# Performance work log

Hardware: AMD Instinct MI355X
Metric: run time of the kernel (lower is better)

Reference implementation:

```python
import jax, jax.numpy as jnp
import numpy as np
import math

D, H, F = 1024, 16, 4096
DH = D // H
EPS_LN = 1e-5


def _layernorm(x, scale, bias):
    mu = jnp.mean(x, axis=-1, keepdims=True)
    var = jnp.mean(jnp.square(x - mu), axis=-1, keepdims=True)
    return (x - mu) * jax.lax.rsqrt(var + EPS_LN) * scale + bias


def setup_inputs() -> dict:
    key = jax.random.key(0)
    ks = jax.random.split(key, 16)
    B, T = 2, 2048
    src = jax.random.normal(ks[0], (B, T, D), dtype=jnp.float32)
    attn_mask = jax.random.randint(ks[1], (T, T), 0, 2) == 1  # bool [T,S], True = masked
    xavier = lambda k, shp: jax.random.uniform(k, shp, jnp.float32, -1.0, 1.0) * math.sqrt(6.0 / (shp[0] + shp[1]))
    return {
        "src": src, "attn_mask": attn_mask,
        "q_w": xavier(ks[2], (D, D)), "q_b": jnp.zeros((D,), jnp.float32),
        "k_w": xavier(ks[3], (D, D)), "k_b": jnp.zeros((D,), jnp.float32),
        "v_w": xavier(ks[4], (D, D)), "v_b": jnp.zeros((D,), jnp.float32),
        "o_w": xavier(ks[5], (D, D)), "o_b": jnp.zeros((D,), jnp.float32),
        "l1_w": xavier(ks[6], (F, D)), "l1_b": jnp.zeros((F,), jnp.float32),
        "l2_w": xavier(ks[7], (D, F)), "l2_b": jnp.zeros((D,), jnp.float32),
        "n1_s": jnp.ones((D,), jnp.float32), "n1_b": jnp.zeros((D,), jnp.float32),
        "n2_s": jnp.ones((D,), jnp.float32), "n2_b": jnp.zeros((D,), jnp.float32),
        "alpha_attn": jax.random.normal(ks[8], (), jnp.float32) * 0.1,
        "alpha_ff": jax.random.normal(ks[9], (), jnp.float32) * 0.1,
    }


def reference(src, attn_mask, q_w, q_b, k_w, k_b, v_w, v_b, o_w, o_b,
              l1_w, l1_b, l2_w, l2_b, n1_s, n1_b, n2_s, n2_b,
              alpha_attn, alpha_ff):
    B, T, _ = src.shape
    # --- self-attention block (post-norm layer, dropout=0 => identity) ---
    q = (src @ q_w.T + q_b).reshape(B, T, H, DH).transpose(0, 2, 1, 3)  # [B,H,T,DH]
    k = (src @ k_w.T + k_b).reshape(B, T, H, DH).transpose(0, 2, 1, 3)
    v = (src @ v_w.T + v_b).reshape(B, T, H, DH).transpose(0, 2, 1, 3)
    scores = jnp.einsum('bhtd,bhsd->bhts', q, k) / math.sqrt(DH)  # [B,H,T,S]
    scores = jnp.where(attn_mask[None, None, :, :], -jnp.inf, scores)
    probs = jax.nn.softmax(scores + 1e-9, axis=-1)
    probs = jnp.where(jnp.isinf(scores), 0.0, probs)  # zero where masked (custom semantics)
    attn = jnp.einsum('bhts,bhsd->bhtd', probs, v).transpose(0, 2, 1, 3).reshape(B, T, D)
    attn = attn @ o_w.T + o_b
    x = _layernorm(src + alpha_attn * attn, n1_s, n1_b)
    # --- FFN block ---
    ff = jax.nn.relu(x @ l1_w.T + l1_b) @ l2_w.T + l2_b
    x = _layernorm(x + alpha_ff * ff, n2_s, n2_b)
    return x
```

## Files before the change

### kernel.cpp

```cpp
#include <hip/hip_runtime.h>
#include <math.h>

#define Dm 1024
#define Hh 16
#define DHd 64
#define Ff 4096
#define Tt 2048
#define Bb 2

#define ATT_C2 0.18033688011112042f

typedef __bf16 bf16_8 __attribute__((ext_vector_type(8)));
typedef __bf16 bf16x2 __attribute__((ext_vector_type(2)));
typedef __bf16 bf16x4 __attribute__((ext_vector_type(4)));
typedef float  f32x4  __attribute__((ext_vector_type(4)));
typedef float  f32x16 __attribute__((ext_vector_type(16)));
typedef unsigned int u32x4 __attribute__((ext_vector_type(4)));
typedef unsigned int u32x8s __attribute__((ext_vector_type(8)));

__device__ __forceinline__ unsigned short f2bf(float f) {
    unsigned int u = __float_as_uint(f);
    unsigned int r = (u + 0x7fffu + ((u >> 16) & 1u)) >> 16;
    return (unsigned short)r;
}

__device__ __forceinline__ bf16x2 pkbf(float a, float b) {
#if __has_builtin(__builtin_amdgcn_cvt_pk_bf16_f32)
    return __builtin_amdgcn_cvt_pk_bf16_f32(a, b);
#else
    bf16x2 r; r[0] = (__bf16)a; r[1] = (__bf16)b; return r;
#endif
}
__device__ __forceinline__ bf16x4 pkbf4(float a, float b, float c, float d) {
    bf16x2 lo = pkbf(a, b), hi = pkbf(c, d);
    return __builtin_shufflevector(lo, hi, 0, 1, 2, 3);
}

__device__ __forceinline__ void plswap32(unsigned &a, unsigned &b) {
#if __has_builtin(__builtin_amdgcn_permlane32_swap)
    auto r = __builtin_amdgcn_permlane32_swap((int)a, (int)b, false, false);
    a = (unsigned)r[0]; b = (unsigned)r[1];
#else
    asm volatile("v_permlane32_swap_b32 %0, %1" : "+v"(a), "+v"(b));
#endif
}

__device__ __forceinline__ void gld_lds16(const void* g, void* l) {
    __builtin_amdgcn_global_load_lds(
        (const __attribute__((address_space(1))) void*)g,
        (__attribute__((address_space(3))) void*)l,
        16, 0, 0);
}

__device__ __forceinline__ void sload32(const unsigned* p,
        u32x8s &a, u32x8s &b, u32x8s &c, u32x8s &d) {
    asm volatile(
        "s_load_dwordx8 %0, %4, 0x0\n\t"
        "s_load_dwordx8 %1, %4, 0x20\n\t"
        "s_load_dwordx8 %2, %4, 0x40\n\t"
        "s_load_dwordx8 %3, %4, 0x60\n\t"
        "s_waitcnt lgkmcnt(0)"
        : "=s"(a), "=s"(b), "=s"(c), "=s"(d)
        : "s"(p));
}

__device__ __forceinline__ float selkeep(float e, unsigned long long keep) {
    float r;
    asm("v_cndmask_b32 %0, 0, %1, %2" : "=v"(r) : "v"(e), "s"(keep));
    return r;
}

__global__ __launch_bounds__(256) void preprocess_kernel(
    const float* __restrict__ q_w, const float* __restrict__ k_w,
    const float* __restrict__ v_w, const float* __restrict__ o_w,
    const float* __restrict__ l1_w, const float* __restrict__ l2_w,
    const float* __restrict__ src, const int* __restrict__ mask,
    const float* __restrict__ q_b, const float* __restrict__ k_b,
    unsigned short* __restrict__ qkw, unsigned short* __restrict__ vw16,
    unsigned short* __restrict__ ow,  unsigned short* __restrict__ l1w,
    unsigned short* __restrict__ l2w, unsigned short* __restrict__ srcb,
    unsigned* __restrict__ mbT, float* __restrict__ qkb)
{
    const int bid = blockIdx.x;
    const int tid = threadIdx.x;
    if (bid < 16384) {
        int i = bid * 256 + tid;
        const float* sp; unsigned short* dp; int off;
        if (i < 1048576) {
            if (i < 262144)      { sp = q_w; dp = qkw;           off = i; }
            else if (i < 524288) { sp = k_w; dp = qkw + 1048576; off = i - 262144; }
            else if (i < 786432) { sp = v_w; dp = vw16;          off = i - 524288; }
            else                 { sp = o_w; dp = ow;            off = i - 786432; }
        } else if (i < 2097152)  { sp = l1_w; dp = l1w;          off = i - 1048576; }
        else if (i < 3145728)    { sp = l2_w; dp = l2w;          off = i - 2097152; }
        else                     { sp = src;  dp = srcb;         off = i - 3145728; }
        float4 v = ((const float4*)sp)[off];
        ((bf16x4*)dp)[off] = pkbf4(v.x, v.y, v.z, v.w);
    } else if (bid < 16896) {
        int w = (bid - 16384) * 256 + tid;
        int tw32 = w >> 11, s = w & 2047;
        const int* p = mask + (size_t)(tw32 * 32) * 2048 + s;
        unsigned bits = 0;
        #pragma unroll
        for (int j = 0; j < 32; ++j)
            bits |= (p[(size_t)j * 2048] == 0 ? 1u : 0u) << j;
        mbT[w] = bits;
    } else {
        int i = (bid - 16896) * 256 + tid;
        qkb[i] = (i < 1024) ? q_b[i] : k_b[i - 1024];
    }
}

template<int RELU, int BF16OUT>
__global__ __launch_bounds__(256) void gemm_bf16_kernel(
    const unsigned short* __restrict__ A, const unsigned short* __restrict__ W,
    const float* __restrict__ bias, void* __restrict__ C, void* __restrict__ C2,
    int M, int N, int K, int ldc, int ksub)
{
    __shared__ __bf16 As[128][64];
    __shared__ __bf16 Bs[128][64];
    const int tid  = threadIdx.x;
    const int lane = tid & 63;
    const int wave = tid >> 6;
    const int m0 = blockIdx.y * 128;
    const int n0 = blockIdx.x * 128;
    const int lr8 = lane >> 3;
    const int gch = (lane & 7) ^ lr8;
    const int wm = (wave & 1) * 64;
    const int wn = (wave >> 1) * 64;
    const int quad = lane >> 4;
    const int lm = lane & 15;
    const int z  = blockIdx.z;
    const int kstart = z * ksub;
    void* Cz = (z == 0) ? C : C2;

    f32x4 acc[4][4];
    #pragma unroll
    for (int i = 0; i < 4; i++)
        #pragma unroll
        for (int j = 0; j < 4; j++) {
            acc[i][j][0] = 0.f; acc[i][j][1] = 0.f;
            acc[i][j][2] = 0.f; acc[i][j][3] = 0.f;
        }

    for (int k0 = kstart; k0 < kstart + ksub; k0 += 64) {
        __syncthreads();
        #pragma unroll
        for (int i = 0; i < 4; i++) {
            int seg = wave * 4 + i;
            int r = seg * 8 + lr8;
            gld_lds16(A + (size_t)(m0 + r) * K + k0 + gch * 8, &As[seg * 8][0]);
            gld_lds16(W + (size_t)(n0 + r) * K + k0 + gch * 8, &Bs[seg * 8][0]);
        }
        __syncthreads();
        #pragma unroll
        for (int kh = 0; kh < 2; kh++) {
            bf16_8 af[4], bfr[4];
            #pragma unroll
            for (int t = 0; t < 4; t++) {
                int ch = (kh * 4 + quad) ^ (lm & 7);
                af[t]  = *(const bf16_8*)&As[wm + t * 16 + lm][ch * 8];
                bfr[t] = *(const bf16_8*)&Bs[wn + t * 16 + lm][ch * 8];
            }
            #pragma unroll
            for (int i = 0; i < 4; i++)
                #pragma unroll
                for (int j = 0; j < 4; j++)
                    acc[i][j] = __builtin_amdgcn_mfma_f32_16x16x32_bf16(
                        af[i], bfr[j], acc[i][j], 0, 0, 0);
        }
    }

    float bvc[4];
    #pragma unroll
    for (int j = 0; j < 4; j++)
        bvc[j] = (z == 0) ? bias[n0 + wn + j * 16 + lm] : 0.f;

    #pragma unroll
    for (int i = 0; i < 4; i++)
        #pragma unroll
        for (int j = 0; j < 4; j++) {
            int col = n0 + wn + j * 16 + lm;
            #pragma unroll
            for (int r = 0; r < 4; r++) {
                int row = m0 + wm + i * 16 + quad * 4 + r;
                float v = acc[i][j][r] + bvc[j];
                if (RELU) v = fmaxf(v, 0.f);
                if (BF16OUT)
                    ((unsigned short*)Cz)[(size_t)row * ldc + col] = f2bf(v);
                else
                    ((float*)Cz)[(size_t)row * ldc + col] = v;
            }
        }
}

__global__ __launch_bounds__(256, 2) void gemm_ffn1_kernel(
    const unsigned short* __restrict__ A, const unsigned short* __restrict__ W,
    const float* __restrict__ bias, unsigned short* __restrict__ C)
{
    __shared__ __bf16 As[256][64];
    __shared__ __bf16 Bs[128][64];
    const int tid  = threadIdx.x;
    const int lane = tid & 63;
    const int wave = tid >> 6;
    const int m0 = blockIdx.y * 256;
    const int n0 = blockIdx.x * 128;
    const int lr8 = lane >> 3;
    const int gch = (lane & 7) ^ lr8;
    const int quad = lane >> 4;
    const int lm = lane & 15;

    f32x4 acc[4][8];
    #pragma unroll
    for (int i = 0; i < 4; i++)
        #pragma unroll
        for (int j = 0; j < 8; j++) {
            acc[i][j][0] = 0.f; acc[i][j][1] = 0.f;
            acc[i][j][2] = 0.f; acc[i][j][3] = 0.f;
        }

    for (int k0 = 0; k0 < 1024; k0 += 64) {
        __syncthreads();
        #pragma unroll
        for (int i = 0; i < 8; i++) {
            int seg = wave * 8 + i;
            int r = seg * 8 + lr8;
            gld_lds16(A + (size_t)(m0 + r) * 1024 + k0 + gch * 8, &As[seg * 8][0]);
        }
        #pragma unroll
        for (int i = 0; i < 4; i++) {
            int seg = wave * 4 + i;
            int r = seg * 8 + lr8;
            gld_lds16(W + (size_t)(n0 + r) * 1024 + k0 + gch * 8, &Bs[seg * 8][0]);
        }
        __syncthreads();
        #pragma unroll
        for (int kh = 0; kh < 2; kh++) {
            const int ch = (kh * 4 + quad) ^ (lm & 7);
            bf16_8 af[4], bfr[8];
            #pragma unroll
            for (int t = 0; t < 4; t++)
                af[t] = *(const bf16_8*)&As[wave * 64 + t * 16 + lm][ch * 8];
            #pragma unroll
            for (int j = 0; j < 8; j++)
                bfr[j] = *(const bf16_8*)&Bs[j * 16 + lm][ch * 8];
            #pragma unroll
            for (int i = 0; i < 4; i++)
                #pragma unroll
                for (int j = 0; j < 8; j++)
                    acc[i][j] = __builtin_amdgcn_mfma_f32_16x16x32_bf16(
                        af[i], bfr[j], acc[i][j], 0, 0, 0);
        }
    }

    float bv[8];
    #pragma unroll
    for (int j = 0; j < 8; j++) bv[j] = bias[n0 + j * 16 + lm];

    #pragma unroll
    for (int i = 0; i < 4; i++)
        #pragma unroll
        for (int j = 0; j < 8; j++) {
            int col = n0 + j * 16 + lm;
            #pragma unroll
            for (int r = 0; r < 4; r++) {
                int row = m0 + wave * 64 + i * 16 + quad * 4 + r;
                float v = fmaxf(acc[i][j][r] + bv[j], 0.f);
                C[(size_t)row * Ff + col] = f2bf(v);
            }
        }
}

__global__ __launch_bounds__(256) void gemm_qkvt_kernel(
    const unsigned short* __restrict__ srcb, const unsigned short* __restrict__ qkw,
    const unsigned short* __restrict__ vw16, const float* __restrict__ qkb,
    const float* __restrict__ v_b,
    unsigned short* __restrict__ qk16, unsigned short* __restrict__ vtf)
{
    const int bid = blockIdx.x;
    const unsigned short *A, *W;
    const float* bias;
    unsigned short* C;
    int m0, n0, ldc;
    bool qscale, rowbias;
    if (bid < 512) {
        A = srcb; W = qkw; bias = qkb; C = qk16;
        n0 = (bid & 15) * 128; m0 = (bid >> 4) * 128;
        ldc = 2048; qscale = true; rowbias = false;
    } else {
        int b2 = bid - 512;
        A = vw16; W = srcb; bias = v_b; C = vtf;
        n0 = (b2 & 31) * 128; m0 = (b2 >> 5) * 128;
        ldc = 4096; qscale = false; rowbias = true;
    }
    const int K = 1024;

    __shared__ __bf16 As[128][64];
    __shared__ __bf16 Bs[128][64];
    const int tid  = threadIdx.x;
    const int lane = tid & 63;
    const int wave = tid >> 6;
    const int lr8 = lane >> 3;
    const int gch = (lane & 7) ^ lr8;
    const int wm = (wave & 1) * 64;
    const int wn = (wave >> 1) * 64;
    const int quad = lane >> 4;
    const int lm = lane & 15;

    f32x4 acc[4][4];
    #pragma unroll
    for (int i = 0; i < 4; i++)
        #pragma unroll
        for (int j = 0; j < 4; j++) {
            acc[i][j][0] = 0.f; acc[i][j][1] = 0.f;
            acc[i][j][2] = 0.f; acc[i][j][3] = 0.f;
        }

    for (int k0 = 0; k0 < K; k0 += 64) {
        __syncthreads();
        #pragma unroll
        for (int i = 0; i < 4; i++) {
            int seg = wave * 4 + i;
            int r = seg * 8 + lr8;
            gld_lds16(A + (size_t)(m0 + r) * K + k0 + gch * 8, &As[seg * 8][0]);
            gld_lds16(W + (size_t)(n0 + r) * K + k0 + gch * 8, &Bs[seg * 8][0]);
        }
        __syncthreads();
        #pragma unroll
        for (int kh = 0; kh < 2; kh++) {
            bf16_8 af[4], bfr[4];
            #pragma unroll
            for (int t = 0; t < 4; t++) {
                int ch = (kh * 4 + quad) ^ (lm & 7);
                af[t]  = *(const bf16_8*)&As[wm + t * 16 + lm][ch * 8];
                bfr[t] = *(const bf16_8*)&Bs[wn + t * 16 + lm][ch * 8];
            }
            #pragma unroll
            for (int i = 0; i < 4; i++)
                #pragma unroll
                for (int j = 0; j < 4; j++)
                    acc[i][j] = __builtin_amdgcn_mfma_f32_16x16x32_bf16(
                        af[i], bfr[j], acc[i][j], 0, 0, 0);
        }
    }

    float bvc[4];
    float brr[4][4];
    if (!rowbias) {
        #pragma unroll
        for (int j = 0; j < 4; j++) bvc[j] = bias[n0 + wn + j * 16 + lm];
    } else {
        #pragma unroll
        for (int i = 0; i < 4; i++) {
            float4 t4 = *(const float4*)&bias[m0 + wm + i * 16 + quad * 4];
            brr[i][0] = t4.x; brr[i][1] = t4.y; brr[i][2] = t4.z; brr[i][3] = t4.w;
        }
    }

    #pragma unroll
    for (int i = 0; i < 4; i++)
        #pragma unroll
        for (int j = 0; j < 4; j++) {
            int col = n0 + wn + j * 16 + lm;
            #pragma unroll
            for (int r = 0; r < 4; r++) {
                int row = m0 + wm + i * 16 + quad * 4 + r;
                float v = acc[i][j][r] + (rowbias ? brr[i][r] : bvc[j]);
                if (qscale && col < 1024) v *= ATT_C2;
                C[(size_t)row * ldc + col] = f2bf(v);
            }
        }
}

__global__ __launch_bounds__(256) void attn_mfma_kernel(
    const unsigned short* __restrict__ qk,
    const unsigned short* __restrict__ vt,
    const unsigned* __restrict__ mbT,
    unsigned short* __restrict__ out)
{
    __shared__ __bf16 Ks[2][128 * 64];
    __shared__ __bf16 Vt[2][64 * 128];

    const int tid  = threadIdx.x;
    const int lane = tid & 63;
    const int wave = tid >> 6;
    const int l31  = lane & 31;
    const int hi   = lane >> 5;
    const int x7   = l31 & 7;
    const int bh = blockIdx.y;
    const int b = bh >> 4, h = bh & 15;
    const int tw = blockIdx.x * 128 + wave * 32;
    const int wvu = __builtin_amdgcn_readfirstlane(wave);
    const unsigned* mrow = mbT + (size_t)(blockIdx.x * 4 + wvu) * 2048;

    bf16_8 qf[4];
    #pragma unroll
    for (int ds4 = 0; ds4 < 4; ++ds4)
        qf[ds4] = *(const bf16_8*)(qk +
            (size_t)(b * Tt + tw + l31) * 2048 + h * DHd + ds4 * 16 + hi * 8);

    f32x16 oacc[2];
    f32x16 ol;
    f32x16 z16;
    #pragma unroll
    for (int r = 0; r < 16; ++r) {
        oacc[0][r] = 0.f; oacc[1][r] = 0.f; ol[r] = 0.f; z16[r] = 0.f;
    }
    bf16_8 vone;
    {
        __bf16 one = (__bf16)1.0f;
        #pragma unroll
        for (int j = 0; j < 8; ++j) vone[j] = one;
    }

    const int krow8 = lane >> 3;
    const int kj    = (lane & 7) ^ krow8;
    const int vr4   = lane >> 4;

    auto STAGE = [&](int nb, int s0) {
        #pragma unroll
        for (int i = 0; i < 4; ++i) {
            int ci = wave * 4 + i;
            {
                int r = 8 * ci + krow8;
                const unsigned short* g = qk +
                    (size_t)(b * Tt + s0 + r) * 2048 + 1024 + h * DHd + kj * 8;
                gld_lds16(g, &Ks[nb][ci * 512]);
            }
            {
                int d = 4 * ci + vr4;
                int jj = (lane & 15) ^ (d & 7);
                const unsigned short* g = vt +
                    (size_t)(h * DHd + d) * 4096 + b * Tt + s0 + jj * 8;
                gld_lds16(g, &Vt[nb][ci * 512]);
            }
        }
    };

    STAGE(0, 0);

    for (int st = 0; st < 16; ++st) {
        const int cb = st & 1;
        const int s0 = st * 128;
        __syncthreads();

        if (st < 15) STAGE(cb ^ 1, s0 + 128);

        #pragma unroll
        for (int sb = 0; sb < 4; ++sb) {
            u32x8s ma, mbw, mc, md;
            sload32(mrow + s0 + sb * 32, ma, mbw, mc, md);

            f32x16 sacc = z16;
            #pragma unroll
            for (int ds4 = 0; ds4 < 4; ++ds4) {
                bf16_8 kf = *(const bf16_8*)&Ks[cb][
                    (sb * 32 + l31) * 64 + (((ds4 * 2 + hi) ^ x7) * 8)];
                sacc = __builtin_amdgcn_mfma_f32_32x32x16_bf16(
                    kf, qf[ds4], sacc, 0, 0, 0);
            }
            float p[16];
            #pragma unroll
            for (int g = 0; g < 4; ++g) {
                u32x8s vv = (g == 0) ? ma : (g == 1) ? mbw : (g == 2) ? mc : md;
                #pragma unroll
                for (int m = 0; m < 4; ++m) {
                    const int reg = g * 4 + m;
                    unsigned long long keep =
                        ((unsigned long long)vv[m + 4] << 32) |
                        (unsigned long long)vv[m];
                    float e = __builtin_amdgcn_exp2f(sacc[reg]);
                    p[reg] = selkeep(e, keep);
                }
            }
            unsigned u[4], v[4];
            #pragma unroll
            for (int g = 0; g < 4; ++g) {
                u[g] = __builtin_bit_cast(unsigned, pkbf(p[g * 4 + 0], p[g * 4 + 1]));
                v[g] = __builtin_bit_cast(unsigned, pkbf(p[g * 4 + 2], p[g * 4 + 3]));
            }
            plswap32(u[0], u[1]); plswap32(v[0], v[1]);
            plswap32(u[2], u[3]); plswap32(v[2], v[3]);
            u32x4 w0; w0[0] = u[0]; w0[1] = v[0]; w0[2] = u[1]; w0[3] = v[1];
            u32x4 w1; w1[0] = u[2]; w1[1] = v[2]; w1[2] = u[3]; w1[3] = v[3];
            bf16_8 pa0 = __builtin_bit_cast(bf16_8, w0);
            bf16_8 pa1 = __builtin_bit_cast(bf16_8, w1);
            #pragma unroll
            for (int kst = 0; kst < 2; ++kst) {
                bf16_8 pa = kst ? pa1 : pa0;
                #pragma unroll
                for (int dblk = 0; dblk < 2; ++dblk) {
                    int cpos = (sb * 4 + kst * 2 + hi) ^ x7;
                    bf16_8 vf = *(const bf16_8*)&Vt[cb][
                        ((dblk * 32 + l31) * 16 + cpos) * 8];
                    oacc[dblk] = __builtin_amdgcn_mfma_f32_32x32x16_bf16(
                        pa, vf, oacc[dblk], 0, 0, 0);
                }
                ol = __builtin_amdgcn_mfma_f32_32x32x16_bf16(
                    pa, vone, ol, 0, 0, 0);
            }
        }
    }

    #pragma unroll
    for (int g = 0; g < 4; ++g)
        #pragma unroll
        for (int m = 0; m < 4; ++m) {
            const int reg = g * 4 + m;
            const int tr = m + 8 * g + 4 * hi;
            float l = ol[reg];
            float inv = (l > 0.f) ? 1.f / l : 0.f;
            int row = b * Tt + tw + tr;
            #pragma unroll
            for (int dblk = 0; dblk < 2; ++dblk)
                out[(size_t)row * Dm + h * DHd + dblk * 32 + l31] =
                    f2bf(oacc[dblk][reg] * inv);
        }
}

template<int NPARTS, int BASEBF, int OUTF32, int OUTBF>
__global__ __launch_bounds__(256) void residual_ln_kernel(
    const void* __restrict__ base, const float* __restrict__ d0,
    const float* __restrict__ d1,
    const float* __restrict__ alpha_p, const float* __restrict__ scale,
    const float* __restrict__ bias, float* __restrict__ out,
    unsigned short* __restrict__ out_bf)
{
    const int row = blockIdx.x;
    const int tid = threadIdx.x;
    const float alpha = alpha_p[0];
    float4 xb;
    if (BASEBF) {
        bf16x4 bb = ((const bf16x4*)((const unsigned short*)base + (size_t)row * Dm))[tid];
        xb.x = (float)bb[0]; xb.y = (float)bb[1]; xb.z = (float)bb[2]; xb.w = (float)bb[3];
    } else {
        xb = ((const float4*)((const float*)base + (size_t)row * Dm))[tid];
    }
    float4 xd = ((const float4*)(d0 + (size_t)row * Dm))[tid];
    if (NPARTS == 2) {
        float4 x2 = ((const float4*)(d1 + (size_t)row * Dm))[tid];
        xd.x += x2.x; xd.y += x2.y; xd.z += x2.z; xd.w += x2.w;
    }
    float4 x;
    x.x = xb.x + alpha * xd.x;
    x.y = xb.y + alpha * xd.y;
    x.z = xb.z + alpha * xd.z;
    x.w = xb.w + alpha * xd.w;
    float s  = x.x + x.y + x.z + x.w;
    float sq = x.x*x.x + x.y*x.y + x.z*x.z + x.w*x.w;
    #pragma unroll
    for (int off = 32; off > 0; off >>= 1) {
        s  += __shfl_down(s, off, 64);
        sq += __shfl_down(sq, off, 64);
    }
    __shared__ float red[8];
    const int w = tid >> 6;
    if ((tid & 63) == 0) { red[w] = s; red[4 + w] = sq; }
    __syncthreads();
    s  = red[0] + red[1] + red[2] + red[3];
    sq = red[4] + red[5] + red[6] + red[7];
    const float mu  = s * (1.f / Dm);
    const float var = sq * (1.f / Dm) - mu * mu;
    const float r   = rsqrtf(var + 1e-5f);
    float4 sc = ((const float4*)scale)[tid];
    float4 bi = ((const float4*)bias)[tid];
    float4 o;
    o.x = (x.x - mu) * r * sc.x + bi.x;
    o.y = (x.y - mu) * r * sc.y + bi.y;
    o.z = (x.z - mu) * r * sc.z + bi.z;
    o.w = (x.w - mu) * r * sc.w + bi.w;
    if (OUTF32)
        ((float4*)(out + (size_t)row * Dm))[tid] = o;
    if (OUTBF)
        ((bf16x4*)(out_bf + (size_t)row * Dm))[tid] = pkbf4(o.x, o.y, o.z, o.w);
}

extern "C" void kernel_launch(void* const* d_in, const int* in_sizes, int n_in,
                              void* d_out, int out_size, void* d_ws, size_t ws_size,
                              hipStream_t stream)
{
    (void)in_sizes; (void)n_in; (void)out_size; (void)ws_size;
    const float* src  = (const float*)d_in[0];
    const int*   mask = (const int*)  d_in[1];
    const float* q_w  = (const float*)d_in[2];
    const float* q_b  = (const float*)d_in[3];
    const float* k_w  = (const float*)d_in[4];
    const float* k_b  = (const float*)d_in[5];
    const float* v_w  = (const float*)d_in[6];
    const float* v_b  = (const float*)d_in[7];
    const float* o_w  = (const float*)d_in[8];
    const float* o_b  = (const float*)d_in[9];
    const float* l1_w = (const float*)d_in[10];
    const float* l1_b = (const float*)d_in[11];
    const float* l2_w = (const float*)d_in[12];
    const float* l2_b = (const float*)d_in[13];
    const float* n1_s = (const float*)d_in[14];
    const float* n1_b = (const float*)d_in[15];
    const float* n2_s = (const float*)d_in[16];
    const float* n2_b = (const float*)d_in[17];
    const float* a_attn = (const float*)d_in[18];
    const float* a_ff   = (const float*)d_in[19];

    const size_t MB = 1024 * 1024;
    char* w = (char*)d_ws;
    unsigned short* qkw  = (unsigned short*)(w + 0);
    unsigned short* vw16 = (unsigned short*)(w + 4  * MB);
    unsigned short* ow   = (unsigned short*)(w + 6  * MB);
    unsigned short* l1w  = (unsigned short*)(w + 8  * MB);
    unsigned short* l2w  = (unsigned short*)(w + 16 * MB);
    unsigned short* srcb = (unsigned short*)(w + 24 * MB);
    unsigned short* qk16 = (unsigned short*)(w + 32 * MB);
    unsigned short* vtf  = (unsigned short*)(w + 48 * MB);
    unsigned*       mbT  = (unsigned*)      (w + 56 * MB);
    float*          qkb  = (float*)         (w + 56 * MB + 524288);
    unsigned short* atb  = (unsigned short*)(w + 24 * MB);
    float*          o0   = (float*)         (w + 58 * MB);
    float*          o1   = (float*)         (w + 74 * MB);
    unsigned short* x1b  = (unsigned short*)(w + 48 * MB);
    unsigned short* hb   = (unsigned short*)(w + 58 * MB);
    float*          fp0  = (float*)         (w + 0);
    float*          fp1  = (float*)         (w + 32 * MB);

    const int MR = Bb * Tt;
    dim3 blk(256);

    preprocess_kernel<<<dim3(16904), blk, 0, stream>>>(
        q_w, k_w, v_w, o_w, l1_w, l2_w, src, mask, q_b, k_b,
        qkw, vw16, ow, l1w, l2w, srcb, mbT, qkb);
    gemm_qkvt_kernel<<<dim3(768), blk, 0, stream>>>(
        srcb, qkw, vw16, qkb, v_b, qk16, vtf);
    attn_mfma_kernel<<<dim3(16, 32), blk, 0, stream>>>(qk16, vtf, mbT, atb);
    gemm_bf16_kernel<0, 0><<<dim3(8, 32, 2), blk, 0, stream>>>(
        atb, ow, o_b, o0, o1, MR, Dm, Dm, Dm, 512);
    residual_ln_kernel<2, 0, 0, 1><<<dim3(MR), blk, 0, stream>>>(
        src, o0, o1, a_attn, n1_s, n1_b, nullptr, x1b);
    gemm_ffn1_kernel<<<dim3(32, 16), blk, 0, stream>>>(x1b, l1w, l1_b, hb);
    gemm_bf16_kernel<0, 0><<<dim3(8, 32, 2), blk, 0, stream>>>(
        hb, l2w, l2_b, fp0, fp1, MR, Dm, Ff, Dm, Ff / 2);
    residual_ln_kernel<2, 1, 1, 0><<<dim3(MR), blk, 0, stream>>>(
        x1b, fp0, fp1, a_ff, n2_s, n2_b, (float*)d_out, nullptr);
}
```

Measured before the change: 376.9 us.

## Split attention key blocks across two wave groups with LDS reduction

```diff
diff --git a/kernel.cpp b/kernel.cpp
--- a/kernel.cpp
+++ b/kernel.cpp
@@ -60,7 +60,7 @@
         "s_load_dwordx8 %2, %4, 0x40\n\t"
         "s_load_dwordx8 %3, %4, 0x60\n\t"
         "s_waitcnt lgkmcnt(0)"
-        : "=s"(a), "=s"(b), "=s"(c), "=s"(d)
+        : "=&s"(a), "=&s"(b), "=&s"(c), "=&s"(d)
         : "s"(p));
 }
 
@@ -372,14 +372,15 @@
         }
 }
 
-__global__ __launch_bounds__(256) void attn_mfma_kernel(
+__global__ __launch_bounds__(512, 4) void attn_mfma_kernel(
     const unsigned short* __restrict__ qk,
     const unsigned short* __restrict__ vt,
     const unsigned* __restrict__ mbT,
     unsigned short* __restrict__ out)
 {
-    __shared__ __bf16 Ks[2][128 * 64];
-    __shared__ __bf16 Vt[2][64 * 128];
+    __shared__ __align__(16) char smem[65536];
+    __bf16* KsP = (__bf16*)smem;
+    __bf16* VtP = (__bf16*)(smem + 32768);
 
     const int tid  = threadIdx.x;
     const int lane = tid & 63;
@@ -389,9 +390,11 @@
     const int x7   = l31 & 7;
     const int bh = blockIdx.y;
     const int b = bh >> 4, h = bh & 15;
-    const int tw = blockIdx.x * 128 + wave * 32;
     const int wvu = __builtin_amdgcn_readfirstlane(wave);
-    const unsigned* mrow = mbT + (size_t)(blockIdx.x * 4 + wvu) * 2048;
+    const int wq  = wvu & 3;
+    const int sh  = wvu >> 2;
+    const int tw = blockIdx.x * 128 + wq * 32;
+    const unsigned* mrow = mbT + (size_t)(blockIdx.x * 4 + wq) * 2048;
 
     bf16_8 qf[4];
     #pragma unroll
@@ -419,20 +422,20 @@
 
     auto STAGE = [&](int nb, int s0) {
         #pragma unroll
-        for (int i = 0; i < 4; ++i) {
-            int ci = wave * 4 + i;
+        for (int i = 0; i < 2; ++i) {
+            int ci = wave * 2 + i;
             {
                 int r = 8 * ci + krow8;
                 const unsigned short* g = qk +
                     (size_t)(b * Tt + s0 + r) * 2048 + 1024 + h * DHd + kj * 8;
-                gld_lds16(g, &Ks[nb][ci * 512]);
+                gld_lds16(g, &KsP[nb * 8192 + ci * 512]);
             }
             {
                 int d = 4 * ci + vr4;
                 int jj = (lane & 15) ^ (d & 7);
                 const unsigned short* g = vt +
                     (size_t)(h * DHd + d) * 4096 + b * Tt + s0 + jj * 8;
-                gld_lds16(g, &Vt[nb][ci * 512]);
+                gld_lds16(g, &VtP[nb * 8192 + ci * 512]);
             }
         }
     };
@@ -447,14 +450,15 @@
         if (st < 15) STAGE(cb ^ 1, s0 + 128);
 
         #pragma unroll
-        for (int sb = 0; sb < 4; ++sb) {
+        for (int sbl = 0; sbl < 2; ++sbl) {
+            const int sb = sh * 2 + sbl;
             u32x8s ma, mbw, mc, md;
             sload32(mrow + s0 + sb * 32, ma, mbw, mc, md);
 
             f32x16 sacc = z16;
             #pragma unroll
             for (int ds4 = 0; ds4 < 4; ++ds4) {
-                bf16_8 kf = *(const bf16_8*)&Ks[cb][
+                bf16_8 kf = *(const bf16_8*)&KsP[cb * 8192 +
                     (sb * 32 + l31) * 64 + (((ds4 * 2 + hi) ^ x7) * 8)];
                 sacc = __builtin_amdgcn_mfma_f32_32x32x16_bf16(
                     kf, qf[ds4], sacc, 0, 0, 0);
@@ -491,7 +495,7 @@
                 #pragma unroll
                 for (int dblk = 0; dblk < 2; ++dblk) {
                     int cpos = (sb * 4 + kst * 2 + hi) ^ x7;
-                    bf16_8 vf = *(const bf16_8*)&Vt[cb][
+                    bf16_8 vf = *(const bf16_8*)&VtP[cb * 8192 +
                         ((dblk * 32 + l31) * 16 + cpos) * 8];
                     oacc[dblk] = __builtin_amdgcn_mfma_f32_32x32x16_bf16(
                         pa, vf, oacc[dblk], 0, 0, 0);
@@ -502,20 +506,57 @@
         }
     }
 
-    #pragma unroll
-    for (int g = 0; g < 4; ++g)
-        #pragma unroll
-        for (int m = 0; m < 4; ++m) {
-            const int reg = g * 4 + m;
-            const int tr = m + 8 * g + 4 * hi;
-            float l = ol[reg];
-            float inv = (l > 0.f) ? 1.f / l : 0.f;
-            int row = b * Tt + tw + tr;
-            #pragma unroll
-            for (int dblk = 0; dblk < 2; ++dblk)
-                out[(size_t)row * Dm + h * DHd + dblk * 32 + l31] =
-                    f2bf(oacc[dblk][reg] * inv);
-        }
+    __syncthreads();
+    float* comb = (float*)smem;
+    if (sh == 1) {
+        #pragma unroll
+        for (int dblk = 0; dblk < 2; ++dblk)
+            #pragma unroll
+            for (int q = 0; q < 4; ++q) {
+                float4 v4 = { oacc[dblk][q * 4 + 0], oacc[dblk][q * 4 + 1],
+                              oacc[dblk][q * 4 + 2], oacc[dblk][q * 4 + 3] };
+                *(float4*)&comb[wq * 3072 + (dblk * 4 + q) * 256 + lane * 4] = v4;
+            }
+        #pragma unroll
+        for (int q = 0; q < 4; ++q) {
+            float4 v4 = { ol[q * 4 + 0], ol[q * 4 + 1],
+                          ol[q * 4 + 2], ol[q * 4 + 3] };
+            *(float4*)&comb[wq * 3072 + (8 + q) * 256 + lane * 4] = v4;
+        }
+    }
+    __syncthreads();
+    if (sh == 0) {
+        #pragma unroll
+        for (int dblk = 0; dblk < 2; ++dblk)
+            #pragma unroll
+            for (int q = 0; q < 4; ++q) {
+                float4 v4 = *(const float4*)&comb[
+                    wq * 3072 + (dblk * 4 + q) * 256 + lane * 4];
+                oacc[dblk][q * 4 + 0] += v4.x; oacc[dblk][q * 4 + 1] += v4.y;
+                oacc[dblk][q * 4 + 2] += v4.z; oacc[dblk][q * 4 + 3] += v4.w;
+            }
+        #pragma unroll
+        for (int q = 0; q < 4; ++q) {
+            float4 v4 = *(const float4*)&comb[
+                wq * 3072 + (8 + q) * 256 + lane * 4];
+            ol[q * 4 + 0] += v4.x; ol[q * 4 + 1] += v4.y;
+            ol[q * 4 + 2] += v4.z; ol[q * 4 + 3] += v4.w;
+        }
+        #pragma unroll
+        for (int g = 0; g < 4; ++g)
+            #pragma unroll
+            for (int m = 0; m < 4; ++m) {
+                const int reg = g * 4 + m;
+                const int tr = m + 8 * g + 4 * hi;
+                float l = ol[reg];
+                float inv = (l > 0.f) ? 1.f / l : 0.f;
+                int row = b * Tt + tw + tr;
+                #pragma unroll
+                for (int dblk = 0; dblk < 2; ++dblk)
+                    out[(size_t)row * Dm + h * DHd + dblk * 32 + l31] =
+                        f2bf(oacc[dblk][reg] * inv);
+            }
+    }
 }
 
 template<int NPARTS, int BASEBF, int OUTF32, int OUTBF>
@@ -629,7 +670,7 @@
         qkw, vw16, ow, l1w, l2w, srcb, mbT, qkb);
     gemm_qkvt_kernel<<<dim3(768), blk, 0, stream>>>(
         srcb, qkw, vw16, qkb, v_b, qk16, vtf);
-    attn_mfma_kernel<<<dim3(16, 32), blk, 0, stream>>>(qk16, vtf, mbT, atb);
+    attn_mfma_kernel<<<dim3(16, 32), dim3(512), 0, stream>>>(qk16, vtf, mbT, atb);
     gemm_bf16_kernel<0, 0><<<dim3(8, 32, 2), blk, 0, stream>>>(
         atb, ow, o_b, o0, o1, MR, Dm, Dm, Dm, 512);
     residual_ln_kernel<2, 0, 0, 1><<<dim3(MR), blk, 0, stream>>>(
```

Result: faster. 356.3 us (-5.5%).
